# Performance work log

Measured on AMD Instinct MI355X. Metric: run time of the kernel, lower is better.

## Reference

```python
import jax, jax.numpy as jnp
from jax import lax
import numpy as np

LOWEST_HZ = 1.0
HIGHEST_HZ = 40.0
FS = 256
ORDER = 5


def _butter_sos(order, cutoff, btype, fs):
    """Butterworth digital filter as second-order sections (scipy-equivalent math)."""
    Wn = cutoff / (0.5 * fs)
    fs2 = 2.0
    warped = 2.0 * fs2 * np.tan(np.pi * Wn / fs2)  # pre-warped analog cutoff
    m = np.arange(1, order + 1)
    p = np.exp(1j * np.pi * (2 * m + order - 1) / (2.0 * order))  # analog prototype poles
    if btype == 'lp':
        z = np.zeros(0, dtype=complex)
        p = p * warped
        k = warped ** order
    else:  # 'hp' : lp2hp transform
        k = 1.0 / np.real(np.prod(-p))
        p = warped / p
        z = np.zeros(order, dtype=complex)
    # bilinear transform (internal fs = 2)
    f2 = 2.0 * fs2
    pd = (f2 + p) / (f2 - p)
    zd = (f2 + z) / (f2 - z)
    kd = k * np.real(np.prod(f2 - z) / np.prod(f2 - p))
    zd = np.concatenate([zd, -np.ones(order - len(zd))])  # pad zeros at z=-1
    z0 = float(np.real(zd[0]))  # all digital zeros identical (z=-1 for lp, z=+1 for hp)
    real_p = [float(pp.real) for pp in pd if abs(pp.imag) < 1e-10]
    cplx_p = [pp for pp in pd if pp.imag > 1e-10]
    sos = []
    for pp in cplx_p:  # conjugate pair -> one biquad
        sos.append([1.0, -2.0 * z0, z0 * z0, 1.0, -2.0 * pp.real, float(np.real(pp * np.conj(pp)))])
    for pr in real_p:  # leftover real pole -> first-order section
        sos.append([1.0, -z0, 0.0, 1.0, -pr, 0.0])
    sos = np.array(sos, dtype=np.float64)
    sos[0, :3] *= kd  # fold overall gain into first section
    return sos


def _sosfilt(sos, x):
    """Cascaded biquad IIR (direct form II transposed), zero initial state. x: [..., T]."""
    S = sos.shape[0]
    b0, b1, b2 = sos[:, 0], sos[:, 1], sos[:, 2]
    a1, a2 = sos[:, 4], sos[:, 5]
    xT = jnp.moveaxis(x, -1, 0)  # [T, ...]
    state0 = jnp.zeros((S, 2) + xT.shape[1:], x.dtype)

    def step(state, xt):
        cur = xt
        new = []
        for i in range(S):  # fixed small cascade of 6 sections
            w1, w2 = state[i, 0], state[i, 1]
            y = b0[i] * cur + w1
            nw1 = b1[i] * cur - a1[i] * y + w2
            nw2 = b2[i] * cur - a2[i] * y
            new.append(jnp.stack([nw1, nw2]))
            cur = y
        return jnp.stack(new), cur

    _, yT = lax.scan(step, state0, xT)
    return jnp.moveaxis(yT, 0, -1)


def setup_inputs() -> dict:
    key = jax.random.key(0)
    x = jax.random.normal(key, (32, 64, 16384), dtype=jnp.float32)
    sos_hp = _butter_sos(ORDER, LOWEST_HZ, 'hp', FS)
    sos_lp = _butter_sos(ORDER, HIGHEST_HZ, 'lp', FS)
    sos = jnp.asarray(np.concatenate([sos_hp, sos_lp], axis=0), dtype=jnp.float32)  # [6,6]
    return {"x": x, "sos": sos}


def reference(x, sos):
    # highpass sections then lowpass sections = one 6-section cascade
    return _sosfilt(sos, x)
```

## Files before the change

### kernel.cpp

```cpp
#include <hip/hip_runtime.h>

#define T_LEN 16384
#define NSEC 6
#define NSTATE 12
#define NMAT (NSTATE * NSTATE)
#define NPOW 8
#define NTHR 512
#define NS_TOT 2048

__device__ __forceinline__ float rfl(float v) {
    return __int_as_float(__builtin_amdgcn_readfirstlane(__float_as_int(v)));
}
__device__ __forceinline__ int swz(int f) {
    return (f & ~15) | ((f ^ (f >> 4)) & 15);
}

__global__ void __launch_bounds__(NTHR, 4)
k_main(const float* __restrict__ x, const float* __restrict__ sos,
       float* __restrict__ y) {
    __shared__ float  Mp[NPOW][NMAT];
    __shared__ double Ad[NMAT];
    __shared__ float4 sm4[1664];
    float* cb = (float*)sm4;

    const int k = threadIdx.x;
    const int t = k & 255;
    const int h = k >> 8;
    const int sig0 = blockIdx.x * 2;

    float b0[NSEC], b1[NSEC], b2[NSEC], a1[NSEC], a2[NSEC];
#pragma unroll
    for (int i = 0; i < NSEC; ++i) {
        b0[i] = rfl(sos[i * 6 + 0]);
        b1[i] = rfl(sos[i * 6 + 1]);
        b2[i] = rfl(sos[i * 6 + 2]);
        a1[i] = rfl(sos[i * 6 + 4]);
        a2[i] = rfl(sos[i * 6 + 5]);
    }

    if (k < NSTATE) {
        float w1[NSEC], w2[NSEC];
#pragma unroll
        for (int i = 0; i < NSEC; ++i) {
            w1[i] = (k == 2 * i) ? 1.f : 0.f;
            w2[i] = (k == 2 * i + 1) ? 1.f : 0.f;
        }
        float cur = 0.f;
#pragma unroll
        for (int i = 0; i < NSEC; ++i) {
            float yv = fmaf(b0[i], cur, w1[i]);
            float n1 = fmaf(b1[i], cur, fmaf(-a1[i], yv, w2[i]));
            float n2 = fmaf(b2[i], cur, -(a2[i] * yv));
            w1[i] = n1; w2[i] = n2; cur = yv;
        }
#pragma unroll
        for (int i = 0; i < NSEC; ++i) {
            Ad[(2 * i) * NSTATE + k]     = (double)w1[i];
            Ad[(2 * i + 1) * NSTATE + k] = (double)w2[i];
        }
    }
    __syncthreads();
    {
        const int rr = k / NSTATE, cc = k % NSTATE;
        for (int it = 1; it <= 13; ++it) {
            double v = 0.0;
            if (k < NMAT) {
#pragma unroll
                for (int kk = 0; kk < NSTATE; ++kk)
                    v = fma(Ad[rr * NSTATE + kk], Ad[kk * NSTATE + cc], v);
            }
            __syncthreads();
            if (k < NMAT) {
                Ad[rr * NSTATE + cc] = v;
                if (it >= 6) Mp[it - 6][k] = (float)v;
            }
            __syncthreads();
        }
    }

    float4 stash[16];
#pragma unroll 1
    for (int r = 0; r < 8; ++r) {
        const int hr = r >> 2, c = r & 3;
        const float4* src = (const float4*)(x + (size_t)(sig0 + hr) * T_LEN + (c << 12));
        float4 v0 = src[k];
        float4 v1 = src[k + 512];
        __syncthreads();
        sm4[swz(k)]       = v0;
        sm4[swz(k + 512)] = v1;
        __syncthreads();
        if (h == hr && (t >> 6) == c) {
            const int tp = t & 63;
#pragma unroll
            for (int m = 0; m < 16; ++m)
                stash[m] = sm4[tp * 16 + (m ^ (tp & 15))];
        }
    }

    float w1_[NSEC], w2_[NSEC];
#pragma unroll
    for (int i = 0; i < NSEC; ++i) { w1_[i] = 0.f; w2_[i] = 0.f; }

    auto fstep = [&](float cur) -> float {
#pragma unroll
        for (int i = 0; i < NSEC; ++i) {
            float yv = fmaf(b0[i], cur, w1_[i]);
            w1_[i] = fmaf(b1[i], cur, fmaf(-a1[i], yv, w2_[i]));
            w2_[i] = fmaf(b2[i], cur, -(a2[i] * yv));
            cur = yv;
        }
        return cur;
    };

#pragma unroll
    for (int m = 0; m < 16; ++m) {
        float4 v = stash[m];
        fstep(v.x); fstep(v.y); fstep(v.z); fstep(v.w);
    }
    float c0[NSTATE];
#pragma unroll
    for (int i = 0; i < NSEC; ++i) { c0[2 * i] = w1_[i]; c0[2 * i + 1] = w2_[i]; }

    __syncthreads();
#pragma unroll 1
    for (int rnd = 0; rnd < NPOW; ++rnd) {
        const int d = 1 << rnd;
#pragma unroll
        for (int j = 0; j < NSTATE; ++j) cb[k * 13 + j] = c0[j];
        __syncthreads();
        if (t >= d) {
            float pr[NSTATE], nc[NSTATE];
#pragma unroll
            for (int j = 0; j < NSTATE; ++j) pr[j] = cb[(k - d) * 13 + j];
#pragma unroll
            for (int q = 0; q < NSTATE; ++q) {
                float acc = c0[q];
#pragma unroll
                for (int kk = 0; kk < NSTATE; ++kk)
                    acc = fmaf(Mp[rnd][q * NSTATE + kk], pr[kk], acc);
                nc[q] = acc;
            }
#pragma unroll
            for (int j = 0; j < NSTATE; ++j) c0[j] = nc[j];
        }
        __syncthreads();
    }
#pragma unroll
    for (int j = 0; j < NSTATE; ++j) cb[k * 13 + j] = c0[j];
    __syncthreads();
#pragma unroll
    for (int i = 0; i < NSEC; ++i) {
        w1_[i] = (t == 0) ? 0.f : cb[(k - 1) * 13 + 2 * i];
        w2_[i] = (t == 0) ? 0.f : cb[(k - 1) * 13 + 2 * i + 1];
    }

#pragma unroll
    for (int m = 0; m < 16; ++m) {
        float4 v = stash[m];
        v.x = fstep(v.x); v.y = fstep(v.y); v.z = fstep(v.z); v.w = fstep(v.w);
        stash[m] = v;
    }

#pragma unroll 1
    for (int r = 0; r < 8; ++r) {
        const int hr = r >> 2, c = r & 3;
        __syncthreads();
        if (h == hr && (t >> 6) == c) {
            const int tp = t & 63;
#pragma unroll
            for (int m = 0; m < 16; ++m)
                sm4[tp * 16 + (m ^ (tp & 15))] = stash[m];
        }
        __syncthreads();
        float4* dst = (float4*)(y + (size_t)(sig0 + hr) * T_LEN + (c << 12));
        dst[k]       = sm4[swz(k)];
        dst[k + 512] = sm4[swz(k + 512)];
    }
}

extern "C" void kernel_launch(void* const* d_in, const int* in_sizes, int n_in,
                              void* d_out, int out_size, void* d_ws, size_t ws_size,
                              hipStream_t stream) {
    const float* x   = (const float*)d_in[0];
    const float* sos = (const float*)d_in[1];
    if (n_in >= 2 && in_sizes[0] <= 256 && in_sizes[1] > 256) {
        x = (const float*)d_in[1];
        sos = (const float*)d_in[0];
    }
    float* out = (float*)d_out;

    int NS = out_size / T_LEN;
    if (NS > NS_TOT) NS = NS_TOT;
    if (NS < 2) NS = 2;

    k_main<<<NS / 2, NTHR, 0, stream>>>(x, sos, out);
}
```

Measured before the change: 118.4 us.

## Precompute matrix powers in separate kernel and use wave-shuffle scan per signal

Moves the 12x12 transition-matrix powering out of every block into a one-block pre-kernel that writes the powers to a global buffer, which each block then copies to shared memory. Each block now handles one signal with 256 threads. The 8-round shared-memory prefix scan with barriers is replaced by a 6-round intra-wave shuffle scan plus a cross-wave fixup using binary matrix powers. Input loads go directly from global into registers instead of through swizzled shared memory. This removes redundant double-precision matrix work and many barriers, at the cost of an extra launch and uncoalesced strided input loads.

```diff
diff --git a/kernel.cpp b/kernel.cpp
--- a/kernel.cpp
+++ b/kernel.cpp
@@ -4,29 +4,82 @@
 #define NSEC 6
 #define NSTATE 12
 #define NMAT (NSTATE * NSTATE)
-#define NPOW 8
-#define NTHR 512
+#define NPOW 6
+#define NTHR 256
 #define NS_TOT 2048
+
+__device__ float g_Mp[NPOW * NMAT];
 
 __device__ __forceinline__ float rfl(float v) {
     return __int_as_float(__builtin_amdgcn_readfirstlane(__float_as_int(v)));
 }
-__device__ __forceinline__ int swz(int f) {
-    return (f & ~15) | ((f ^ (f >> 4)) & 15);
+
+__global__ void k_matpow(const float* __restrict__ sos) {
+    __shared__ double A[NMAT];
+    int tid = threadIdx.x;
+
+    if (tid < NSTATE) {
+        double b0[NSEC], b1[NSEC], b2[NSEC], a1[NSEC], a2[NSEC];
+#pragma unroll
+        for (int i = 0; i < NSEC; ++i) {
+            b0[i] = (double)sos[i * 6 + 0];
+            b1[i] = (double)sos[i * 6 + 1];
+            b2[i] = (double)sos[i * 6 + 2];
+            a1[i] = (double)sos[i * 6 + 4];
+            a2[i] = (double)sos[i * 6 + 5];
+        }
+        double w1[NSEC], w2[NSEC];
+#pragma unroll
+        for (int i = 0; i < NSEC; ++i) {
+            w1[i] = (tid == 2 * i) ? 1.0 : 0.0;
+            w2[i] = (tid == 2 * i + 1) ? 1.0 : 0.0;
+        }
+        double cur = 0.0;
+#pragma unroll
+        for (int i = 0; i < NSEC; ++i) {
+            double yv = fma(b0[i], cur, w1[i]);
+            double n1 = fma(b1[i], cur, fma(-a1[i], yv, w2[i]));
+            double n2 = fma(b2[i], cur, -(a2[i] * yv));
+            w1[i] = n1; w2[i] = n2; cur = yv;
+        }
+#pragma unroll
+        for (int i = 0; i < NSEC; ++i) {
+            A[(2 * i) * NSTATE + tid]     = w1[i];
+            A[(2 * i + 1) * NSTATE + tid] = w2[i];
+        }
+    }
+    __syncthreads();
+    const int rr = tid / NSTATE, cc = tid % NSTATE;
+    for (int it = 1; it <= 11; ++it) {
+        double v = 0.0;
+        if (tid < NMAT) {
+#pragma unroll
+            for (int kk = 0; kk < NSTATE; ++kk)
+                v = fma(A[rr * NSTATE + kk], A[kk * NSTATE + cc], v);
+        }
+        __syncthreads();
+        if (tid < NMAT) {
+            A[rr * NSTATE + cc] = v;
+            if (it >= 6) g_Mp[(it - 6) * NMAT + tid] = (float)v;
+        }
+        __syncthreads();
+    }
 }
 
 __global__ void __launch_bounds__(NTHR, 4)
 k_main(const float* __restrict__ x, const float* __restrict__ sos,
        float* __restrict__ y) {
-    __shared__ float  Mp[NPOW][NMAT];
-    __shared__ double Ad[NMAT];
-    __shared__ float4 sm4[1664];
-    float* cb = (float*)sm4;
+    __shared__ float Mp[NPOW][NMAT];
+    __shared__ float cw[4][NSTATE];
+    __shared__ float4 sm4[1024];
 
     const int k = threadIdx.x;
-    const int t = k & 255;
-    const int h = k >> 8;
-    const int sig0 = blockIdx.x * 2;
+    const int lane = k & 63;
+    const int w = k >> 6;
+    const int sig = blockIdx.x;
+
+    for (int i = k; i < NPOW * NMAT; i += NTHR)
+        Mp[i / NMAT][i % NMAT] = g_Mp[i];
 
     float b0[NSEC], b1[NSEC], b2[NSEC], a1[NSEC], a2[NSEC];
 #pragma unroll
@@ -38,65 +91,8 @@
         a2[i] = rfl(sos[i * 6 + 5]);
     }
 
-    if (k < NSTATE) {
-        float w1[NSEC], w2[NSEC];
-#pragma unroll
-        for (int i = 0; i < NSEC; ++i) {
-            w1[i] = (k == 2 * i) ? 1.f : 0.f;
-            w2[i] = (k == 2 * i + 1) ? 1.f : 0.f;
-        }
-        float cur = 0.f;
-#pragma unroll
-        for (int i = 0; i < NSEC; ++i) {
-            float yv = fmaf(b0[i], cur, w1[i]);
-            float n1 = fmaf(b1[i], cur, fmaf(-a1[i], yv, w2[i]));
-            float n2 = fmaf(b2[i], cur, -(a2[i] * yv));
-            w1[i] = n1; w2[i] = n2; cur = yv;
-        }
-#pragma unroll
-        for (int i = 0; i < NSEC; ++i) {
-            Ad[(2 * i) * NSTATE + k]     = (double)w1[i];
-            Ad[(2 * i + 1) * NSTATE + k] = (double)w2[i];
-        }
-    }
-    __syncthreads();
-    {
-        const int rr = k / NSTATE, cc = k % NSTATE;
-        for (int it = 1; it <= 13; ++it) {
-            double v = 0.0;
-            if (k < NMAT) {
-#pragma unroll
-                for (int kk = 0; kk < NSTATE; ++kk)
-                    v = fma(Ad[rr * NSTATE + kk], Ad[kk * NSTATE + cc], v);
-            }
-            __syncthreads();
-            if (k < NMAT) {
-                Ad[rr * NSTATE + cc] = v;
-                if (it >= 6) Mp[it - 6][k] = (float)v;
-            }
-            __syncthreads();
-        }
-    }
-
+    const float4* xp4 = (const float4*)(x + (size_t)sig * T_LEN) + k * 16;
     float4 stash[16];
-#pragma unroll 1
-    for (int r = 0; r < 8; ++r) {
-        const int hr = r >> 2, c = r & 3;
-        const float4* src = (const float4*)(x + (size_t)(sig0 + hr) * T_LEN + (c << 12));
-        float4 v0 = src[k];
-        float4 v1 = src[k + 512];
-        __syncthreads();
-        sm4[swz(k)]       = v0;
-        sm4[swz(k + 512)] = v1;
-        __syncthreads();
-        if (h == hr && (t >> 6) == c) {
-            const int tp = t & 63;
-#pragma unroll
-            for (int m = 0; m < 16; ++m)
-                stash[m] = sm4[tp * 16 + (m ^ (tp & 15))];
-        }
-    }
-
     float w1_[NSEC], w2_[NSEC];
 #pragma unroll
     for (int i = 0; i < NSEC; ++i) { w1_[i] = 0.f; w2_[i] = 0.f; }
@@ -114,7 +110,8 @@
 
 #pragma unroll
     for (int m = 0; m < 16; ++m) {
-        float4 v = stash[m];
+        float4 v = xp4[m];
+        stash[m] = v;
         fstep(v.x); fstep(v.y); fstep(v.z); fstep(v.w);
     }
     float c0[NSTATE];
@@ -122,16 +119,15 @@
     for (int i = 0; i < NSEC; ++i) { c0[2 * i] = w1_[i]; c0[2 * i + 1] = w2_[i]; }
 
     __syncthreads();
-#pragma unroll 1
-    for (int rnd = 0; rnd < NPOW; ++rnd) {
+
+#pragma unroll
+    for (int rnd = 0; rnd < 6; ++rnd) {
         const int d = 1 << rnd;
-#pragma unroll
-        for (int j = 0; j < NSTATE; ++j) cb[k * 13 + j] = c0[j];
-        __syncthreads();
-        if (t >= d) {
-            float pr[NSTATE], nc[NSTATE];
-#pragma unroll
-            for (int j = 0; j < NSTATE; ++j) pr[j] = cb[(k - d) * 13 + j];
+        float pr[NSTATE];
+#pragma unroll
+        for (int j = 0; j < NSTATE; ++j) pr[j] = __shfl_up(c0[j], d, 64);
+        if (lane >= d) {
+            float nc[NSTATE];
 #pragma unroll
             for (int q = 0; q < NSTATE; ++q) {
                 float acc = c0[q];
@@ -143,16 +139,49 @@
 #pragma unroll
             for (int j = 0; j < NSTATE; ++j) c0[j] = nc[j];
         }
-        __syncthreads();
-    }
-#pragma unroll
-    for (int j = 0; j < NSTATE; ++j) cb[k * 13 + j] = c0[j];
+    }
+
+    if (lane == 63) {
+#pragma unroll
+        for (int j = 0; j < NSTATE; ++j) cw[w][j] = c0[j];
+    }
     __syncthreads();
-#pragma unroll
-    for (int i = 0; i < NSEC; ++i) {
-        w1_[i] = (t == 0) ? 0.f : cb[(k - 1) * 13 + 2 * i];
-        w2_[i] = (t == 0) ? 0.f : cb[(k - 1) * 13 + 2 * i + 1];
-    }
+
+    if (w > 0) {
+        float v[NSTATE];
+#pragma unroll
+        for (int j = 0; j < NSTATE; ++j) v[j] = cw[w - 1][j];
+#pragma unroll
+        for (int i = 0; i < NPOW; ++i) {
+            if (((lane + 1) >> i) & 1) {
+                float nv[NSTATE];
+#pragma unroll
+                for (int q = 0; q < NSTATE; ++q) {
+                    float acc = 0.f;
+#pragma unroll
+                    for (int kk = 0; kk < NSTATE; ++kk)
+                        acc = fmaf(Mp[i][q * NSTATE + kk], v[kk], acc);
+                    nv[q] = acc;
+                }
+#pragma unroll
+                for (int j = 0; j < NSTATE; ++j) v[j] = nv[j];
+            }
+        }
+        if (lane != 63) {
+#pragma unroll
+            for (int j = 0; j < NSTATE; ++j) c0[j] += v[j];
+        }
+    }
+
+    float si[NSTATE];
+#pragma unroll
+    for (int j = 0; j < NSTATE; ++j) si[j] = __shfl_up(c0[j], 1, 64);
+    if (lane == 0) {
+#pragma unroll
+        for (int j = 0; j < NSTATE; ++j) si[j] = (w == 0) ? 0.f : cw[w - 1][j];
+    }
+#pragma unroll
+    for (int i = 0; i < NSEC; ++i) { w1_[i] = si[2 * i]; w2_[i] = si[2 * i + 1]; }
 
 #pragma unroll
     for (int m = 0; m < 16; ++m) {
@@ -161,20 +190,22 @@
         stash[m] = v;
     }
 
+    float4* yp4 = (float4*)(y + (size_t)sig * T_LEN);
 #pragma unroll 1
-    for (int r = 0; r < 8; ++r) {
-        const int hr = r >> 2, c = r & 3;
+    for (int r = 0; r < 4; ++r) {
+        if (w == r) {
+#pragma unroll
+            for (int m = 0; m < 16; ++m)
+                sm4[lane * 16 + (m ^ (lane & 15))] = stash[m];
+        }
         __syncthreads();
-        if (h == hr && (t >> 6) == c) {
-            const int tp = t & 63;
-#pragma unroll
-            for (int m = 0; m < 16; ++m)
-                sm4[tp * 16 + (m ^ (tp & 15))] = stash[m];
-        }
-        __syncthreads();
-        float4* dst = (float4*)(y + (size_t)(sig0 + hr) * T_LEN + (c << 12));
-        dst[k]       = sm4[swz(k)];
-        dst[k + 512] = sm4[swz(k + 512)];
+#pragma unroll
+        for (int q = 0; q < 4; ++q) {
+            int j = k + 256 * q;
+            int s = (j & ~15) | ((j ^ (j >> 4)) & 15);
+            yp4[r * 1024 + j] = sm4[s];
+        }
+        if (r < 3) __syncthreads();
     }
 }
 
@@ -191,7 +222,8 @@
 
     int NS = out_size / T_LEN;
     if (NS > NS_TOT) NS = NS_TOT;
-    if (NS < 2) NS = 2;
-
-    k_main<<<NS / 2, NTHR, 0, stream>>>(x, sos, out);
-}
+    if (NS < 1) NS = 1;
+
+    k_matpow<<<1, 256, 0, stream>>>(sos);
+    k_main<<<NS, NTHR, 0, stream>>>(x, sos, out);
+}
```

After: 107.6 us. -9.1%, faster.
